# Optimization experiments

Hardware: AMD Instinct MI355X
Metric: run time of the kernel (lower is better)

The kernel has to match this reference:

```python
import jax, jax.numpy as jnp
import numpy as np


def _lin_relu(V, W, b):
    # LinearEmbedding: matmul + bias + ReLU (with_act_func=True default)
    return jax.nn.relu(jnp.matmul(V, W) + b)


def setup_inputs() -> dict:
    key = jax.random.key(0)
    ks = jax.random.split(key, 8)
    B, N, F = 4, 4096, 512
    C = F // 8
    sx = 1.0 / np.sqrt(F)
    return {
        "V": jax.random.normal(ks[0], (B, N, F), dtype=jnp.float32),
        "Wf": jax.random.normal(ks[1], (F, C), dtype=jnp.float32) * sx,
        "bf": jax.random.normal(ks[2], (C,), dtype=jnp.float32) * 5e-5 + 1e-4,
        "Wg": jax.random.normal(ks[3], (F, C), dtype=jnp.float32) * sx,
        "bg": jax.random.normal(ks[4], (C,), dtype=jnp.float32) * 5e-5 + 1e-4,
        "Wh": jax.random.normal(ks[5], (F, F), dtype=jnp.float32) * sx,
        "bh": jax.random.normal(ks[6], (F,), dtype=jnp.float32) * 5e-5 + 1e-4,
        "gamma": jax.random.normal(ks[7], (F,), dtype=jnp.float32),
    }


def reference(V, Wf, bf, Wg, bg, Wh, bh, gamma):
    f_out = _lin_relu(V, Wf, bf)          # [B, N, C]
    g_out = _lin_relu(V, Wg, bg)          # [B, N, C]
    h_out = _lin_relu(V, Wh, bh)          # [B, N, F]
    scores = jnp.einsum('bnc,bmc->bnm', f_out, g_out)  # [B, N, N]
    s = jax.nn.softmax(scores, axis=-1)
    o = jnp.einsum('bnm,bmf->bnf', s, h_out)            # [B, N, F]
    return gamma * o + V
```

## Files before the change

kernel.cpp:

```cpp
#include <hip/hip_runtime.h>
#include <hip/hip_bf16.h>
#include <math.h>

#define M_ROWS 16384
#define F_DIM 512
#define C_DIM 64

typedef short bf16x8 __attribute__((ext_vector_type(8)));
typedef float floatx4 __attribute__((ext_vector_type(4)));
typedef unsigned short ushortx8 __attribute__((ext_vector_type(8)));
typedef unsigned short ushortx4 __attribute__((ext_vector_type(4)));

static __device__ __forceinline__ unsigned short f2bf(float x) {
    __hip_bfloat16 h = __float2bfloat16(x);
    return *reinterpret_cast<unsigned short*>(&h);
}
static __device__ __forceinline__ float bf2f(unsigned short h) {
    unsigned int u = ((unsigned int)h) << 16;
    return __builtin_bit_cast(float, u);
}

static __device__ __forceinline__ void lgkm_barrier() {
    asm volatile("s_waitcnt lgkmcnt(0)\n\ts_barrier" ::: "memory");
}


__global__ __launch_bounds__(64) void prep_w_kernel(
    const float* __restrict__ Wf, const float* __restrict__ Wg,
    const float* __restrict__ Wh,
    unsigned short* __restrict__ wt_hi, unsigned short* __restrict__ wt_lo)
{
    const int c = blockIdx.x;
    const int t = threadIdx.x;
    const float* W; int ld, cl;
    if (c < 64)       { W = Wf; ld = C_DIM; cl = c; }
    else if (c < 128) { W = Wg; ld = C_DIM; cl = c - 64; }
    else              { W = Wh; ld = F_DIM; cl = c - 128; }
    const int ng = c >> 4, l16 = c & 15;
    for (int k = t; k < F_DIM; k += 64) {
        const float x = W[(size_t)k * ld + cl];
        const unsigned short h = f2bf(x);
        const int kh = k >> 5, qd = (k >> 3) & 3, j = k & 7;
        const size_t off = (((size_t)(ng * 16 + kh) * 64) + qd * 16 + l16) * 8 + j;
        wt_hi[off] = h;
        wt_lo[off] = f2bf(x - bf2f(h));
    }
}

__global__ __launch_bounds__(256) void conv_v_kernel(
    const float* __restrict__ V,
    unsigned short* __restrict__ v_hi, unsigned short* __restrict__ v_lo)
{
    const int o   = blockIdx.x * 256 + threadIdx.x;
    const int l16 = o & 15, kq = (o >> 4) & 3, kg = (o >> 6) & 15, rg = o >> 10;
    const int row = rg * 16 + l16;
    const int k   = kg * 32 + kq * 8;
    const float4 x0 = *(const float4*)(V + (size_t)row * F_DIM + k);
    const float4 x1 = *(const float4*)(V + (size_t)row * F_DIM + k + 4);
    const float xs[8] = {x0.x, x0.y, x0.z, x0.w, x1.x, x1.y, x1.z, x1.w};
    ushortx8 hi, lo;
    #pragma unroll
    for (int j = 0; j < 8; ++j) {
        const unsigned short h = f2bf(xs[j]);
        hi[j] = h;
        lo[j] = f2bf(xs[j] - bf2f(h));
    }
    *(ushortx8*)(v_hi + (size_t)o * 8) = hi;
    *(ushortx8*)(v_lo + (size_t)o * 8) = lo;
}

#define BM 64

__global__ __launch_bounds__(256, 4) void embed_mfma_kernel(
    const unsigned short* __restrict__ v_hi, const unsigned short* __restrict__ v_lo,
    const unsigned short* __restrict__ wt_hi, const unsigned short* __restrict__ wt_lo,
    const float* __restrict__ bf, const float* __restrict__ bg,
    const float* __restrict__ bh,
    unsigned short* __restrict__ f_bf, unsigned short* __restrict__ g_bf,
    unsigned short* __restrict__ h_sw)
{
    const int t  = threadIdx.x;
    const int q  = blockIdx.x;
    const int yb = blockIdx.y;
    const int R0 = q * BM;
    const bool fg = (yb == 0);
    const int cbase = fg ? 0 : yb * 128;

    const int w = t >> 6, lane = t & 63, quad = lane >> 4, l16 = lane & 15;
    const int ng0 = (cbase >> 4) + w * 2;
    const int rg0 = q * 4;

    floatx4 acc[4][2];
    #pragma unroll
    for (int rt = 0; rt < 4; ++rt)
        #pragma unroll
        for (int c = 0; c < 2; ++c)
            acc[rt][c] = (floatx4){0.f, 0.f, 0.f, 0.f};

    #pragma unroll 2
    for (int kg = 0; kg < 16; ++kg) {
        const bf16x8 b0 = *(const bf16x8*)(wt_hi + (((size_t)(ng0 * 16 + kg)) * 64 + lane) * 8);
        const bf16x8 b1 = *(const bf16x8*)(wt_hi + (((size_t)((ng0 + 1) * 16 + kg)) * 64 + lane) * 8);
        bf16x8 a[4];
        #pragma unroll
        for (int rt = 0; rt < 4; ++rt)
            a[rt] = *(const bf16x8*)(v_hi + (((size_t)(rg0 + rt) * 16 + kg) * 64 + lane) * 8);
        #pragma unroll
        for (int rt = 0; rt < 4; ++rt) {
            acc[rt][0] = __builtin_amdgcn_mfma_f32_16x16x32_bf16(a[rt], b0, acc[rt][0], 0, 0, 0);
            acc[rt][1] = __builtin_amdgcn_mfma_f32_16x16x32_bf16(a[rt], b1, acc[rt][1], 0, 0, 0);
        }
        if (fg) {
            const bf16x8 c0 = *(const bf16x8*)(wt_lo + (((size_t)(ng0 * 16 + kg)) * 64 + lane) * 8);
            const bf16x8 c1 = *(const bf16x8*)(wt_lo + (((size_t)((ng0 + 1) * 16 + kg)) * 64 + lane) * 8);
            bf16x8 al[4];
            #pragma unroll
            for (int rt = 0; rt < 4; ++rt)
                al[rt] = *(const bf16x8*)(v_lo + (((size_t)(rg0 + rt) * 16 + kg) * 64 + lane) * 8);
            #pragma unroll
            for (int rt = 0; rt < 4; ++rt) {
                acc[rt][0] = __builtin_amdgcn_mfma_f32_16x16x32_bf16(a[rt],  c0, acc[rt][0], 0, 0, 0);
                acc[rt][0] = __builtin_amdgcn_mfma_f32_16x16x32_bf16(al[rt], b0, acc[rt][0], 0, 0, 0);
                acc[rt][1] = __builtin_amdgcn_mfma_f32_16x16x32_bf16(a[rt],  c1, acc[rt][1], 0, 0, 0);
                acc[rt][1] = __builtin_amdgcn_mfma_f32_16x16x32_bf16(al[rt], b1, acc[rt][1], 0, 0, 0);
            }
        }
    }

    #pragma unroll
    for (int rt = 0; rt < 4; ++rt) {
        #pragma unroll
        for (int c = 0; c < 2; ++c) {
            const int wtc  = cbase + w * 32 + c * 16 + l16;
            const int rowl = rt * 16 + quad * 4;
            const float bias = fg ? (wtc < 64 ? bf[wtc] : bg[wtc - 64]) : bh[wtc - 128];
            const floatx4 v = acc[rt][c];
            if (fg) {
                unsigned short* dst = (wtc < 64) ? (f_bf + wtc) : (g_bf + wtc - 64);
                #pragma unroll
                for (int r = 0; r < 4; ++r) {
                    const float z = v[r] + bias;
                    dst[(size_t)(R0 + rowl + r) * C_DIM] = f2bf(z > 0.f ? z : 0.f);
                }
            } else {
                const int hc   = wtc - 128;
                const int grow = R0 + rowl;
                const int b    = grow >> 12, rl = grow & 4095;
                const int T    = rl >> 6, mloc = rl & 63;
                const int kh2  = mloc >> 5, q2 = (mloc >> 3) & 3, j0 = mloc & 7;
                ushortx4 st;
                #pragma unroll
                for (int r = 0; r < 4; ++r) {
                    const float z = v[r] + bias;
                    st[r] = f2bf(z > 0.f ? z : 0.f);
                }
                const size_t off = ((((size_t)(b * 64 + T) * 64) + (hc >> 4) * 2 + kh2) * 64
                                    + q2 * 16 + (hc & 15)) * 8 + j0;
                *(ushortx4*)(h_sw + off) = st;
            }
        }
    }
}

#define QT 128

__global__ __launch_bounds__(1024, 4) void attn_mfma_kernel(
    const unsigned short* __restrict__ f_bf, const unsigned short* __restrict__ g_bf,
    const unsigned short* __restrict__ h_sw, const float* __restrict__ gamma,
    const float* __restrict__ V, float* __restrict__ out)
{
    __shared__ __align__(16) unsigned short p_lds[2][QT * 128];
    __shared__ __align__(16) unsigned short g_lds[2][128 * 64];
    __shared__ float l_red[2][QT];
    __shared__ float l_inv[QT];

    const int t = threadIdx.x;
    const int w = t >> 6, lane = t & 63, quad = lane >> 4, l16 = lane & 15;
    const int sr = (w & 7) * 16, sc = (w >> 3) * 32;

    const int bid = blockIdx.x;
    const int b   = (bid & 7) >> 1;
    const int ch  = bid & 1;
    const int qb  = bid >> 3;
    const int R0  = qb * QT;

    const unsigned short* fb    = f_bf + ((size_t)b * 4096 + R0) * C_DIM;
    const unsigned short* gb    = g_bf + (size_t)b * 4096 * C_DIM;
    const unsigned short* hbase = h_sw + (size_t)b * 64 * 32768;
    const int hgrp = (ch * 16 + w) * 2;

    bf16x8 f0, f1;
    {
        const unsigned short* fr = fb + (size_t)(sr + l16) * C_DIM + quad * 8;
        f0 = *(const bf16x8*)fr;
        f1 = *(const bf16x8*)(fr + 32);
    }
    const float gam = gamma[ch * 256 + w * 16 + l16];

    floatx4 acc[8];
    #pragma unroll
    for (int rt = 0; rt < 8; ++rt)
        acc[rt] = (floatx4){0.f, 0.f, 0.f, 0.f};
    float run_l[4] = {0.f, 0.f, 0.f, 0.f};

    const int grow    = t >> 3, gc8 = (t & 7) * 8;
    const int g_swoff = grow * 128 + ((gc8 * 2) ^ ((grow & 7) << 4));
    ushortx8 greg = *(const ushortx8*)(gb + (size_t)grow * C_DIM + gc8);

    for (int it = 0; it < 32; ++it) {
        const int buf = it & 1;

        const unsigned short* ht0 = hbase + (size_t)(2 * it) * 32768 + (size_t)hgrp * 512;
        const unsigned short* ht1 = ht0 + 32768;
        const bf16x8 h0 = *(const bf16x8*)(ht0 + (size_t)lane * 8);
        const bf16x8 h1 = *(const bf16x8*)(ht0 + 512 + (size_t)lane * 8);
        const bf16x8 h2 = *(const bf16x8*)(ht1 + (size_t)lane * 8);
        const bf16x8 h3 = *(const bf16x8*)(ht1 + 512 + (size_t)lane * 8);

        *(ushortx8*)((unsigned char*)&g_lds[buf][0] + g_swoff) = greg;
        if (it < 31)
            greg = *(const ushortx8*)(gb + (size_t)((it + 1) * 128 + grow) * C_DIM + gc8);
        lgkm_barrier();

        const unsigned char* gB = (const unsigned char*)&g_lds[buf][0];
        unsigned char*       pB = (unsigned char*)&p_lds[buf][0];

        #pragma unroll
        for (int sct = 0; sct < 4; ++sct) {
            const int s = sct >> 1, ct = sct & 1;
            const int srow = s * 64 + sc + ct * 16 + l16;
            const int sgw  = (srow & 7) << 4;
            const bf16x8 g0 = *(const bf16x8*)(gB + srow * 128 + ((quad * 16)      ^ sgw));
            const bf16x8 g1 = *(const bf16x8*)(gB + srow * 128 + ((quad * 16 + 64) ^ sgw));
            floatx4 cc = (floatx4){0.f, 0.f, 0.f, 0.f};
            cc = __builtin_amdgcn_mfma_f32_16x16x32_bf16(f0, g0, cc, 0, 0, 0);
            cc = __builtin_amdgcn_mfma_f32_16x16x32_bf16(f1, g1, cc, 0, 0, 0);
            #pragma unroll
            for (int r = 0; r < 4; ++r) {
                const float p = __expf(cc[r] - 32.f);
                run_l[r] += p;
                const int prow = sr + quad * 4 + r;
                const int bcol = (s * 64 + sc + ct * 16 + l16) * 2;
                *(unsigned short*)(pB + prow * 256 + (bcol ^ ((prow & 7) << 4))) = f2bf(p);
            }
        }
        lgkm_barrier();

        #pragma unroll
        for (int rt = 0; rt < 8; ++rt) {
            const int prow = rt * 16 + l16;
            const int sw   = (prow & 7) << 4;
            const unsigned char* pr = pB + prow * 256;
            const bf16x8 pf0 = *(const bf16x8*)(pr + ((quad * 16)       ^ sw));
            const bf16x8 pf1 = *(const bf16x8*)(pr + ((quad * 16 + 64)  ^ sw));
            const bf16x8 pf2 = *(const bf16x8*)(pr + ((quad * 16 + 128) ^ sw));
            const bf16x8 pf3 = *(const bf16x8*)(pr + ((quad * 16 + 192) ^ sw));
            acc[rt] = __builtin_amdgcn_mfma_f32_16x16x32_bf16(pf0, h0, acc[rt], 0, 0, 0);
            acc[rt] = __builtin_amdgcn_mfma_f32_16x16x32_bf16(pf1, h1, acc[rt], 0, 0, 0);
            acc[rt] = __builtin_amdgcn_mfma_f32_16x16x32_bf16(pf2, h2, acc[rt], 0, 0, 0);
            acc[rt] = __builtin_amdgcn_mfma_f32_16x16x32_bf16(pf3, h3, acc[rt], 0, 0, 0);
        }
    }

    #pragma unroll
    for (int r = 0; r < 4; ++r) {
        float v = run_l[r];
        v += __shfl_xor(v, 1, 64);
        v += __shfl_xor(v, 2, 64);
        v += __shfl_xor(v, 4, 64);
        v += __shfl_xor(v, 8, 64);
        if (l16 == 0) l_red[w >> 3][sr + quad * 4 + r] = v;
    }
    __syncthreads();
    if (t < QT)
        l_inv[t] = 1.f / (l_red[0][t] + l_red[1][t]);
    __syncthreads();

    const float* Vb = V   + ((size_t)b * 4096 + R0) * F_DIM;
    float*       ob = out + ((size_t)b * 4096 + R0) * F_DIM;
    const int col = ch * 256 + w * 16 + l16;
    #pragma unroll
    for (int rt = 0; rt < 8; ++rt) {
        #pragma unroll
        for (int r = 0; r < 4; ++r) {
            const int row = rt * 16 + quad * 4 + r;
            ob[(size_t)row * F_DIM + col] =
                gam * acc[rt][r] * l_inv[row] + Vb[(size_t)row * F_DIM + col];
        }
    }
}

extern "C" void kernel_launch(void* const* d_in, const int* in_sizes, int n_in,
                              void* d_out, int out_size, void* d_ws, size_t ws_size,
                              hipStream_t stream) {
    const float* V     = (const float*)d_in[0];
    const float* Wf    = (const float*)d_in[1];
    const float* bf    = (const float*)d_in[2];
    const float* Wg    = (const float*)d_in[3];
    const float* bg    = (const float*)d_in[4];
    const float* Wh    = (const float*)d_in[5];
    const float* bh    = (const float*)d_in[6];
    const float* gamma = (const float*)d_in[7];
    float* out = (float*)d_out;

    unsigned short* f_bf  = (unsigned short*)d_ws;
    unsigned short* g_bf  = f_bf + (size_t)M_ROWS * C_DIM;
    unsigned short* h_sw  = g_bf + (size_t)M_ROWS * C_DIM;
    unsigned short* wt_hi = h_sw + (size_t)4 * F_DIM * 4096;
    unsigned short* wt_lo = wt_hi + (size_t)640 * F_DIM;
    unsigned short* v_hi  = wt_lo + (size_t)640 * F_DIM;
    unsigned short* v_lo  = v_hi + (size_t)M_ROWS * F_DIM;

    conv_v_kernel<<<M_ROWS * F_DIM / 8 / 256, 256, 0, stream>>>(V, v_hi, v_lo);
    prep_w_kernel<<<640, 64, 0, stream>>>(Wf, Wg, Wh, wt_hi, wt_lo);
    embed_mfma_kernel<<<dim3(256, 5), 256, 0, stream>>>(
        v_hi, v_lo, wt_hi, wt_lo, bf, bg, bh, f_bf, g_bf, h_sw);
    attn_mfma_kernel<<<256, 1024, 0, stream>>>(f_bf, g_bf, h_sw, gamma, V, out);
}
```

Measured before the change: 247.0 us.

## Retile embed and attention kernels: 64-row query blocks covering all columns

The embedding kernel moves from 4x2 to 2x4 row/column tiles per wave, so each wave loads fewer V fragments and more weight fragments. The attention kernel now gives each block 64 query rows across all 512 output columns, where before it used 128 rows split over two column-halves. Each K tile is split into two 64-row halves, the score work is spread over a 4x4 wave grid, and blocks are remapped for batch locality. This removes the duplicated score and exp computation that both column-half blocks used to repeat, at the cost of more h fragment loads per wave and a four-way row-sum reduction.

Result: faster. 218.1 us (-11.7%).

```diff
diff --git a/kernel.cpp b/kernel.cpp
--- a/kernel.cpp
+++ b/kernel.cpp
@@ -87,52 +87,50 @@
     const int cbase = fg ? 0 : yb * 128;
 
     const int w = t >> 6, lane = t & 63, quad = lane >> 4, l16 = lane & 15;
-    const int ng0 = (cbase >> 4) + w * 2;
-    const int rg0 = q * 4;
-
-    floatx4 acc[4][2];
-    #pragma unroll
-    for (int rt = 0; rt < 4; ++rt)
-        #pragma unroll
-        for (int c = 0; c < 2; ++c)
+    const int wr = w & 1, wcol = w >> 1;
+    const int ng0 = (cbase >> 4) + wcol * 4;
+    const int rg0 = q * 4 + wr * 2;
+
+    floatx4 acc[2][4];
+    #pragma unroll
+    for (int rt = 0; rt < 2; ++rt)
+        #pragma unroll
+        for (int c = 0; c < 4; ++c)
             acc[rt][c] = (floatx4){0.f, 0.f, 0.f, 0.f};
 
     #pragma unroll 2
     for (int kg = 0; kg < 16; ++kg) {
-        const bf16x8 b0 = *(const bf16x8*)(wt_hi + (((size_t)(ng0 * 16 + kg)) * 64 + lane) * 8);
-        const bf16x8 b1 = *(const bf16x8*)(wt_hi + (((size_t)((ng0 + 1) * 16 + kg)) * 64 + lane) * 8);
-        bf16x8 a[4];
-        #pragma unroll
-        for (int rt = 0; rt < 4; ++rt)
-            a[rt] = *(const bf16x8*)(v_hi + (((size_t)(rg0 + rt) * 16 + kg) * 64 + lane) * 8);
-        #pragma unroll
-        for (int rt = 0; rt < 4; ++rt) {
-            acc[rt][0] = __builtin_amdgcn_mfma_f32_16x16x32_bf16(a[rt], b0, acc[rt][0], 0, 0, 0);
-            acc[rt][1] = __builtin_amdgcn_mfma_f32_16x16x32_bf16(a[rt], b1, acc[rt][1], 0, 0, 0);
+        const bf16x8 a0 = *(const bf16x8*)(v_hi + (((size_t)rg0 * 16 + kg) * 64 + lane) * 8);
+        const bf16x8 a1 = *(const bf16x8*)(v_hi + (((size_t)(rg0 + 1) * 16 + kg) * 64 + lane) * 8);
+        bf16x8 b[4];
+        #pragma unroll
+        for (int c = 0; c < 4; ++c)
+            b[c] = *(const bf16x8*)(wt_hi + (((size_t)(ng0 + c) * 16 + kg) * 64 + lane) * 8);
+        #pragma unroll
+        for (int c = 0; c < 4; ++c) {
+            acc[0][c] = __builtin_amdgcn_mfma_f32_16x16x32_bf16(a0, b[c], acc[0][c], 0, 0, 0);
+            acc[1][c] = __builtin_amdgcn_mfma_f32_16x16x32_bf16(a1, b[c], acc[1][c], 0, 0, 0);
         }
         if (fg) {
-            const bf16x8 c0 = *(const bf16x8*)(wt_lo + (((size_t)(ng0 * 16 + kg)) * 64 + lane) * 8);
-            const bf16x8 c1 = *(const bf16x8*)(wt_lo + (((size_t)((ng0 + 1) * 16 + kg)) * 64 + lane) * 8);
-            bf16x8 al[4];
+            const bf16x8 a0l = *(const bf16x8*)(v_lo + (((size_t)rg0 * 16 + kg) * 64 + lane) * 8);
+            const bf16x8 a1l = *(const bf16x8*)(v_lo + (((size_t)(rg0 + 1) * 16 + kg) * 64 + lane) * 8);
             #pragma unroll
-            for (int rt = 0; rt < 4; ++rt)
-                al[rt] = *(const bf16x8*)(v_lo + (((size_t)(rg0 + rt) * 16 + kg) * 64 + lane) * 8);
-            #pragma unroll
-            for (int rt = 0; rt < 4; ++rt) {
-                acc[rt][0] = __builtin_amdgcn_mfma_f32_16x16x32_bf16(a[rt],  c0, acc[rt][0], 0, 0, 0);
-                acc[rt][0] = __builtin_amdgcn_mfma_f32_16x16x32_bf16(al[rt], b0, acc[rt][0], 0, 0, 0);
-                acc[rt][1] = __builtin_amdgcn_mfma_f32_16x16x32_bf16(a[rt],  c1, acc[rt][1], 0, 0, 0);
-                acc[rt][1] = __builtin_amdgcn_mfma_f32_16x16x32_bf16(al[rt], b1, acc[rt][1], 0, 0, 0);
+            for (int c = 0; c < 4; ++c) {
+                const bf16x8 bl = *(const bf16x8*)(wt_lo + (((size_t)(ng0 + c) * 16 + kg) * 64 + lane) * 8);
+                acc[0][c] = __builtin_amdgcn_mfma_f32_16x16x32_bf16(a0,  bl,   acc[0][c], 0, 0, 0);
+                acc[0][c] = __builtin_amdgcn_mfma_f32_16x16x32_bf16(a0l, b[c], acc[0][c], 0, 0, 0);
+                acc[1][c] = __builtin_amdgcn_mfma_f32_16x16x32_bf16(a1,  bl,   acc[1][c], 0, 0, 0);
+                acc[1][c] = __builtin_amdgcn_mfma_f32_16x16x32_bf16(a1l, b[c], acc[1][c], 0, 0, 0);
             }
         }
     }
 
     #pragma unroll
-    for (int rt = 0; rt < 4; ++rt) {
-        #pragma unroll
-        for (int c = 0; c < 2; ++c) {
-            const int wtc  = cbase + w * 32 + c * 16 + l16;
-            const int rowl = rt * 16 + quad * 4;
+    for (int rt = 0; rt < 2; ++rt) {
+        #pragma unroll
+        for (int c = 0; c < 4; ++c) {
+            const int wtc  = cbase + wcol * 64 + c * 16 + l16;
+            const int rowl = wr * 32 + rt * 16 + quad * 4;
             const float bias = fg ? (wtc < 64 ? bf[wtc] : bg[wtc - 64]) : bh[wtc - 128];
             const floatx4 v = acc[rt][c];
             if (fg) {
@@ -162,76 +160,80 @@
     }
 }
 
-#define QT 128
+#define QT 64
 
 __global__ __launch_bounds__(1024, 4) void attn_mfma_kernel(
     const unsigned short* __restrict__ f_bf, const unsigned short* __restrict__ g_bf,
     const unsigned short* __restrict__ h_sw, const float* __restrict__ gamma,
     const float* __restrict__ V, float* __restrict__ out)
 {
-    __shared__ __align__(16) unsigned short p_lds[2][QT * 128];
-    __shared__ __align__(16) unsigned short g_lds[2][128 * 64];
-    __shared__ float l_red[2][QT];
+    __shared__ __align__(16) unsigned short p_lds[2][2][QT * 64];
+    __shared__ __align__(16) unsigned short g_lds[2][2][64 * 64];
+    __shared__ float l_red[4][QT];
     __shared__ float l_inv[QT];
 
     const int t = threadIdx.x;
     const int w = t >> 6, lane = t & 63, quad = lane >> 4, l16 = lane & 15;
-    const int sr = (w & 7) * 16, sc = (w >> 3) * 32;
-
-    const int bid = blockIdx.x;
-    const int b   = (bid & 7) >> 1;
-    const int ch  = bid & 1;
-    const int qb  = bid >> 3;
-    const int R0  = qb * QT;
+    const int wr = w & 3, wc = w >> 2;
+
+    const int bid  = blockIdx.x;
+    const int orig = (bid & 7) * 32 + (bid >> 3);
+    const int b    = orig >> 6, qb = orig & 63;
+    const int R0   = qb * QT;
 
     const unsigned short* fb    = f_bf + ((size_t)b * 4096 + R0) * C_DIM;
     const unsigned short* gb    = g_bf + (size_t)b * 4096 * C_DIM;
     const unsigned short* hbase = h_sw + (size_t)b * 64 * 32768;
-    const int hgrp = (ch * 16 + w) * 2;
 
     bf16x8 f0, f1;
     {
-        const unsigned short* fr = fb + (size_t)(sr + l16) * C_DIM + quad * 8;
+        const unsigned short* fr = fb + (size_t)(wr * 16 + l16) * C_DIM + quad * 8;
         f0 = *(const bf16x8*)fr;
         f1 = *(const bf16x8*)(fr + 32);
     }
-    const float gam = gamma[ch * 256 + w * 16 + l16];
-
-    floatx4 acc[8];
-    #pragma unroll
-    for (int rt = 0; rt < 8; ++rt)
-        acc[rt] = (floatx4){0.f, 0.f, 0.f, 0.f};
+    const float gam0 = gamma[w * 32 + l16];
+    const float gam1 = gamma[w * 32 + 16 + l16];
+
+    floatx4 acc[4][2];
+    #pragma unroll
+    for (int rt = 0; rt < 4; ++rt)
+        #pragma unroll
+        for (int c = 0; c < 2; ++c)
+            acc[rt][c] = (floatx4){0.f, 0.f, 0.f, 0.f};
     float run_l[4] = {0.f, 0.f, 0.f, 0.f};
 
-    const int grow    = t >> 3, gc8 = (t & 7) * 8;
-    const int g_swoff = grow * 128 + ((gc8 * 2) ^ ((grow & 7) << 4));
-    ushortx8 greg = *(const ushortx8*)(gb + (size_t)grow * C_DIM + gc8);
+    const int grow = t >> 3, gchunk = t & 7;
+    const int ghalf = grow >> 6, gr64 = grow & 63;
+    const int g_swoff = gr64 * 128 + ((gchunk * 16) ^ ((gr64 & 7) << 4));
+    ushortx8 greg = *(const ushortx8*)(gb + (size_t)grow * C_DIM + gchunk * 8);
+
+    const int sgrow   = wc * 16 + l16;
+    const int sg_off0 = sgrow * 128 + ((quad * 16)      ^ ((sgrow & 7) << 4));
+    const int sg_off1 = sgrow * 128 + ((quad * 16 + 64) ^ ((sgrow & 7) << 4));
 
     for (int it = 0; it < 32; ++it) {
         const int buf = it & 1;
 
-        const unsigned short* ht0 = hbase + (size_t)(2 * it) * 32768 + (size_t)hgrp * 512;
+        const unsigned short* ht0 = hbase + (size_t)(2 * it) * 32768 + (size_t)(4 * w) * 512;
         const unsigned short* ht1 = ht0 + 32768;
-        const bf16x8 h0 = *(const bf16x8*)(ht0 + (size_t)lane * 8);
-        const bf16x8 h1 = *(const bf16x8*)(ht0 + 512 + (size_t)lane * 8);
-        const bf16x8 h2 = *(const bf16x8*)(ht1 + (size_t)lane * 8);
-        const bf16x8 h3 = *(const bf16x8*)(ht1 + 512 + (size_t)lane * 8);
-
-        *(ushortx8*)((unsigned char*)&g_lds[buf][0] + g_swoff) = greg;
+        bf16x8 h[2][4];
+        #pragma unroll
+        for (int gi = 0; gi < 4; ++gi) {
+            h[0][gi] = *(const bf16x8*)(ht0 + gi * 512 + (size_t)lane * 8);
+            h[1][gi] = *(const bf16x8*)(ht1 + gi * 512 + (size_t)lane * 8);
+        }
+
+        *(ushortx8*)((unsigned char*)&g_lds[buf][ghalf][0] + g_swoff) = greg;
         if (it < 31)
-            greg = *(const ushortx8*)(gb + (size_t)((it + 1) * 128 + grow) * C_DIM + gc8);
+            greg = *(const ushortx8*)(gb + (size_t)((it + 1) * 128 + grow) * C_DIM + gchunk * 8);
         lgkm_barrier();
 
-        const unsigned char* gB = (const unsigned char*)&g_lds[buf][0];
-        unsigned char*       pB = (unsigned char*)&p_lds[buf][0];
-
-        #pragma unroll
-        for (int sct = 0; sct < 4; ++sct) {
-            const int s = sct >> 1, ct = sct & 1;
-            const int srow = s * 64 + sc + ct * 16 + l16;
-            const int sgw  = (srow & 7) << 4;
-            const bf16x8 g0 = *(const bf16x8*)(gB + srow * 128 + ((quad * 16)      ^ sgw));
-            const bf16x8 g1 = *(const bf16x8*)(gB + srow * 128 + ((quad * 16 + 64) ^ sgw));
+        #pragma unroll
+        for (int s = 0; s < 2; ++s) {
+            const unsigned char* gB = (const unsigned char*)&g_lds[buf][s][0];
+            unsigned char*       pB = (unsigned char*)&p_lds[buf][s][0];
+            const bf16x8 g0 = *(const bf16x8*)(gB + sg_off0);
+            const bf16x8 g1 = *(const bf16x8*)(gB + sg_off1);
             floatx4 cc = (floatx4){0.f, 0.f, 0.f, 0.f};
             cc = __builtin_amdgcn_mfma_f32_16x16x32_bf16(f0, g0, cc, 0, 0, 0);
             cc = __builtin_amdgcn_mfma_f32_16x16x32_bf16(f1, g1, cc, 0, 0, 0);
@@ -239,26 +241,27 @@
             for (int r = 0; r < 4; ++r) {
                 const float p = __expf(cc[r] - 32.f);
                 run_l[r] += p;
-                const int prow = sr + quad * 4 + r;
-                const int bcol = (s * 64 + sc + ct * 16 + l16) * 2;
-                *(unsigned short*)(pB + prow * 256 + (bcol ^ ((prow & 7) << 4))) = f2bf(p);
+                const int prow = wr * 16 + quad * 4 + r;
+                const int pcol = wc * 16 + l16;
+                *(unsigned short*)(pB + prow * 128 + ((pcol * 2) ^ ((prow & 7) << 4))) = f2bf(p);
             }
         }
         lgkm_barrier();
 
         #pragma unroll
-        for (int rt = 0; rt < 8; ++rt) {
+        for (int rt = 0; rt < 4; ++rt) {
             const int prow = rt * 16 + l16;
             const int sw   = (prow & 7) << 4;
-            const unsigned char* pr = pB + prow * 256;
-            const bf16x8 pf0 = *(const bf16x8*)(pr + ((quad * 16)       ^ sw));
-            const bf16x8 pf1 = *(const bf16x8*)(pr + ((quad * 16 + 64)  ^ sw));
-            const bf16x8 pf2 = *(const bf16x8*)(pr + ((quad * 16 + 128) ^ sw));
-            const bf16x8 pf3 = *(const bf16x8*)(pr + ((quad * 16 + 192) ^ sw));
-            acc[rt] = __builtin_amdgcn_mfma_f32_16x16x32_bf16(pf0, h0, acc[rt], 0, 0, 0);
-            acc[rt] = __builtin_amdgcn_mfma_f32_16x16x32_bf16(pf1, h1, acc[rt], 0, 0, 0);
-            acc[rt] = __builtin_amdgcn_mfma_f32_16x16x32_bf16(pf2, h2, acc[rt], 0, 0, 0);
-            acc[rt] = __builtin_amdgcn_mfma_f32_16x16x32_bf16(pf3, h3, acc[rt], 0, 0, 0);
+            #pragma unroll
+            for (int s = 0; s < 2; ++s) {
+                const unsigned char* pB = (const unsigned char*)&p_lds[buf][s][0];
+                const bf16x8 pf0 = *(const bf16x8*)(pB + prow * 128 + ((quad * 16)      ^ sw));
+                const bf16x8 pf1 = *(const bf16x8*)(pB + prow * 128 + ((quad * 16 + 64) ^ sw));
+                acc[rt][0] = __builtin_amdgcn_mfma_f32_16x16x32_bf16(pf0, h[s][0], acc[rt][0], 0, 0, 0);
+                acc[rt][0] = __builtin_amdgcn_mfma_f32_16x16x32_bf16(pf1, h[s][1], acc[rt][0], 0, 0, 0);
+                acc[rt][1] = __builtin_amdgcn_mfma_f32_16x16x32_bf16(pf0, h[s][2], acc[rt][1], 0, 0, 0);
+                acc[rt][1] = __builtin_amdgcn_mfma_f32_16x16x32_bf16(pf1, h[s][3], acc[rt][1], 0, 0, 0);
+            }
         }
     }
 
@@ -269,23 +272,24 @@
         v += __shfl_xor(v, 2, 64);
         v += __shfl_xor(v, 4, 64);
         v += __shfl_xor(v, 8, 64);
-        if (l16 == 0) l_red[w >> 3][sr + quad * 4 + r] = v;
+        if (l16 == 0) l_red[wc][wr * 16 + quad * 4 + r] = v;
     }
     __syncthreads();
     if (t < QT)
-        l_inv[t] = 1.f / (l_red[0][t] + l_red[1][t]);
+        l_inv[t] = 1.f / (l_red[0][t] + l_red[1][t] + l_red[2][t] + l_red[3][t]);
     __syncthreads();
 
     const float* Vb = V   + ((size_t)b * 4096 + R0) * F_DIM;
     float*       ob = out + ((size_t)b * 4096 + R0) * F_DIM;
-    const int col = ch * 256 + w * 16 + l16;
-    #pragma unroll
-    for (int rt = 0; rt < 8; ++rt) {
+    #pragma unroll
+    for (int rt = 0; rt < 4; ++rt) {
         #pragma unroll
         for (int r = 0; r < 4; ++r) {
             const int row = rt * 16 + quad * 4 + r;
-            ob[(size_t)row * F_DIM + col] =
-                gam * acc[rt][r] * l_inv[row] + Vb[(size_t)row * F_DIM + col];
+            const float li = l_inv[row];
+            const int c0 = w * 32 + l16;
+            ob[(size_t)row * F_DIM + c0]      = gam0 * acc[rt][0][r] * li + Vb[(size_t)row * F_DIM + c0];
+            ob[(size_t)row * F_DIM + c0 + 16] = gam1 * acc[rt][1][r] * li + Vb[(size_t)row * F_DIM + c0 + 16];
         }
     }
 }
```
